# Kernel tuning notes

Hardware: AMD Instinct MI355X
Metric: run time of the kernel (lower is better)

The kernel has to match this reference:

```python
import math
import jax, jax.numpy as jnp
import numpy as np

B, T, D = 8, 2048, 512
EPS = 1e-5


def _gate(x, W, b, a, g, beta):
    # Linear -> PReLU (single shared slope a) -> LayerNorm -> sigmoid
    h = x @ W.T + b
    h = jnp.where(h >= 0, h, a * h)
    mu = jnp.mean(h, axis=-1, keepdims=True)
    var = jnp.var(h, axis=-1, keepdims=True)
    h = (h - mu) / jnp.sqrt(var + EPS) * g + beta
    return jax.nn.sigmoid(h)


def setup_inputs() -> dict:
    key = jax.random.key(0)
    ks = jax.random.split(key, 12)
    lin = lambda k: jax.random.normal(k, (D, D), jnp.float32) * 0.02
    z = jnp.zeros((D,), jnp.float32)
    o = jnp.ones((D,), jnp.float32)
    a0 = jnp.float32(0.25)  # PReLU default init
    inp = {
        "query": jax.random.normal(ks[0], (B, T, D), jnp.float32),
        "value": jax.random.normal(ks[1], (B, T, D), jnp.float32),
        "aux_emb": jax.random.normal(ks[2], (B, 1, D), jnp.float32),
        # ragged valid lengths in [T//2, T] to keep every sample realistic
        "input_len": jax.random.randint(ks[3], (B,), T // 2, T + 1),
        "Wq": lin(ks[4]), "bq": z,
        "Wqg": lin(ks[5]), "bqg": z, "aq": a0, "gq": o, "betaq": z,
        "Wkg": lin(ks[6]), "bkg": z, "ak": a0, "gk": o, "betak": z,
        "Wvg": lin(ks[7]), "bvg": z, "av": a0, "gv": o, "betav": z,
        "Wsig": lin(ks[8]), "bsig": z,
        "Wtan": lin(ks[9]), "btan": z,
    }
    return inp


def reference(query, value, aux_emb, input_len,
              Wq, bq,
              Wqg, bqg, aq, gq, betaq,
              Wkg, bkg, ak, gk, betak,
              Wvg, bvg, av, gv, betav,
              Wsig, bsig, Wtan, btan):
    q = query @ Wq.T + bq
    q = q * _gate(aux_emb, Wqg, bqg, aq, gq, betaq)          # [B,T,D]
    k = value * _gate(aux_emb, Wkg, bkg, ak, gk, betak)      # [B,T,D]
    vg = _gate(aux_emb, Wvg, bvg, av, gv, betav)             # [B,1,D]
    vg = jax.nn.sigmoid(vg @ Wsig.T + bsig) * jnp.tanh(vg @ Wtan.T + btan)
    v = value * vg                                           # [B,T,D]

    w = jnp.einsum('btd,bsd->bts', q, k) / math.sqrt(D)      # [B,T,T]
    r = jnp.arange(T)
    causal = (r[:, None] >= r[None, :]).astype(w.dtype)      # tril ones
    w = w * causal
    w = jnp.where(w == 0.0, -jnp.inf, w)  # torch quirk: exact zeros -> -inf
    L = input_len[:, None, None]                              # [B,1,1]
    invalid = (r[None, :, None] < L) & (r[None, None, :] >= L)
    w = jnp.where(invalid, -jnp.inf, w)
    p = jax.nn.softmax(w, axis=-1)
    # rows beyond input_len are padding: zero them (torch code produced NaN
    # there via -inf*0; intended semantics is zeroed padding rows)
    row_valid = (r[None, :, None] < L).astype(p.dtype)        # [B,T,1]
    p = p * row_valid
    return p @ v                                              # [B,T,D]
```

## Files before the change

### kernel.cpp

```cpp
#include <hip/hip_runtime.h>
#include <hip/hip_bf16.h>
#include <stdint.h>

#define BB 8
#define TT 2048
#define DD 512

typedef __attribute__((ext_vector_type(8))) __bf16 bf16x8;
typedef __attribute__((ext_vector_type(4))) float f32x4;

__device__ __forceinline__ unsigned short f2bf(float f) {
    unsigned u = __builtin_bit_cast(unsigned, f);
    unsigned r = u + 0x7fffu + ((u >> 16) & 1u);
    return (unsigned short)(r >> 16);
}

__device__ __forceinline__ void gload_lds16(const unsigned short* g, unsigned short* l) {
    __builtin_amdgcn_global_load_lds(
        (const __attribute__((address_space(1))) void*)g,
        (__attribute__((address_space(3))) void*)l, 16, 0, 0);
}

__global__ __launch_bounds__(256) void gates_mv1(
    const float* __restrict__ aux,
    const float* __restrict__ Wqg, const float* __restrict__ bqg, const float* __restrict__ aq,
    const float* __restrict__ Wkg, const float* __restrict__ bkg, const float* __restrict__ ak,
    const float* __restrict__ Wvg, const float* __restrict__ bvg, const float* __restrict__ av,
    float* __restrict__ h) {
    __shared__ float saux[BB * DD];
    int tid = threadIdx.x;
#pragma unroll
    for (int i = 0; i < 4; i++) {
        int idx = tid + i * 256;
        ((float4*)saux)[idx] = ((const float4*)aux)[idx];
    }
    __syncthreads();
    int wave = (blockIdx.x * 256 + tid) >> 6;
    int lane = tid & 63;
    int g = wave >> 9, r = wave & 511;
    const float* W    = (g == 0) ? Wqg : (g == 1) ? Wkg : Wvg;
    const float* bias = (g == 0) ? bqg : (g == 1) ? bkg : bvg;
    const float* alpha = (g == 0) ? aq : (g == 1) ? ak : av;
    const float4* Wrow = (const float4*)(W + (size_t)r * DD);
    float acc[BB];
#pragma unroll
    for (int b = 0; b < BB; b++) acc[b] = 0.f;
#pragma unroll
    for (int c = 0; c < 2; c++) {
        float4 w4 = Wrow[lane + c * 64];
#pragma unroll
        for (int b = 0; b < BB; b++) {
            float4 a4 = ((const float4*)(saux + b * DD))[lane + c * 64];
            acc[b] += w4.x * a4.x + w4.y * a4.y + w4.z * a4.z + w4.w * a4.w;
        }
    }
#pragma unroll
    for (int b = 0; b < BB; b++) {
#pragma unroll
        for (int s = 1; s < 64; s <<= 1) acc[b] += __shfl_xor(acc[b], s, 64);
    }
    if (lane == 0) {
        float bi = bias[r], a = alpha[0];
#pragma unroll
        for (int b = 0; b < BB; b++) {
            float v = acc[b] + bi;
            v = (v >= 0.f) ? v : a * v;
            h[(g * BB + b) * DD + r] = v;
        }
    }
}

__global__ __launch_bounds__(512) void gates_norm(
    const float* __restrict__ h,
    const float* __restrict__ gq, const float* __restrict__ betaq,
    const float* __restrict__ gk, const float* __restrict__ betak,
    const float* __restrict__ gv, const float* __restrict__ betav,
    float* __restrict__ qgate, float* __restrict__ kgate, float* __restrict__ vg) {
    int g = blockIdx.x >> 3, b = blockIdx.x & 7, tid = threadIdx.x;
    __shared__ float red[DD], red2[DD];
    float hv = h[(g * BB + b) * DD + tid];
    red[tid] = hv; red2[tid] = hv * hv;
    __syncthreads();
    for (int s = 256; s > 0; s >>= 1) {
        if (tid < s) { red[tid] += red[tid + s]; red2[tid] += red2[tid + s]; }
        __syncthreads();
    }
    float mu = red[0] * (1.f / DD);
    float var = red2[0] * (1.f / DD) - mu * mu;
    const float* gg = (g == 0) ? gq : (g == 1) ? gk : gv;
    const float* be = (g == 0) ? betaq : (g == 1) ? betak : betav;
    float val = (hv - mu) * rsqrtf(var + 1e-5f) * gg[tid] + be[tid];
    float sg = 1.f / (1.f + expf(-val));
    float* outp = (g == 0) ? qgate : (g == 1) ? kgate : vg;
    outp[b * DD + tid] = sg;
}

__global__ __launch_bounds__(256) void gates_mv2(
    const float* __restrict__ vg,
    const float* __restrict__ Wsig, const float* __restrict__ bsig,
    const float* __restrict__ Wtan, const float* __restrict__ btan,
    float* __restrict__ vgate) {
    __shared__ float svg[BB * DD];
    int tid = threadIdx.x;
#pragma unroll
    for (int i = 0; i < 4; i++) {
        int idx = tid + i * 256;
        ((float4*)svg)[idx] = ((const float4*)vg)[idx];
    }
    __syncthreads();
    int r = (blockIdx.x * 256 + tid) >> 6;
    int lane = tid & 63;
    const float4* Ws = (const float4*)(Wsig + (size_t)r * DD);
    const float4* Wt = (const float4*)(Wtan + (size_t)r * DD);
    float as_[BB], at_[BB];
#pragma unroll
    for (int b = 0; b < BB; b++) { as_[b] = 0.f; at_[b] = 0.f; }
#pragma unroll
    for (int c = 0; c < 2; c++) {
        float4 w1 = Ws[lane + c * 64];
        float4 w2 = Wt[lane + c * 64];
#pragma unroll
        for (int b = 0; b < BB; b++) {
            float4 a4 = ((const float4*)(svg + b * DD))[lane + c * 64];
            as_[b] += w1.x * a4.x + w1.y * a4.y + w1.z * a4.z + w1.w * a4.w;
            at_[b] += w2.x * a4.x + w2.y * a4.y + w2.z * a4.z + w2.w * a4.w;
        }
    }
#pragma unroll
    for (int b = 0; b < BB; b++) {
#pragma unroll
        for (int s = 1; s < 64; s <<= 1) {
            as_[b] += __shfl_xor(as_[b], s, 64);
            at_[b] += __shfl_xor(at_[b], s, 64);
        }
    }
    if (lane == 0) {
        float b1 = bsig[r], b2 = btan[r];
#pragma unroll
        for (int b = 0; b < BB; b++) {
            float s1 = 1.f / (1.f + expf(-(as_[b] + b1)));
            float s2 = tanhf(at_[b] + b2);
            vgate[b * DD + r] = s1 * s2;
        }
    }
}

__global__ __launch_bounds__(256) void convert_kernel(
    const float* __restrict__ query, const float* __restrict__ Wq,
    const float* __restrict__ value,
    const float* __restrict__ kgate, const float* __restrict__ vgate,
    unsigned short* __restrict__ queryb, unsigned short* __restrict__ Wqb,
    unsigned short* __restrict__ kb, unsigned short* __restrict__ vbT) {
    __shared__ float tile[32][33];
    int bi = blockIdx.x, tid = threadIdx.x;
    if (bi < 8192) {
        int idx = bi * 256 + tid;
        float4 q4 = ((const float4*)query)[idx];
        ushort4 oq;
        oq.x = f2bf(q4.x); oq.y = f2bf(q4.y); oq.z = f2bf(q4.z); oq.w = f2bf(q4.w);
        ((ushort4*)queryb)[idx] = oq;
    } else if (bi < 8448) {
        int idx = (bi - 8192) * 256 + tid;
        float4 w4 = ((const float4*)Wq)[idx];
        ushort4 o;
        o.x = f2bf(w4.x); o.y = f2bf(w4.y); o.z = f2bf(w4.z); o.w = f2bf(w4.w);
        ((ushort4*)Wqb)[idx] = o;
    } else {
        int vb = bi - 8448;
        int tIdx = vb & 63, dIdx = (vb >> 6) & 15, b = vb >> 10;
        int t0 = tIdx * 32, d0 = dIdx * 32;
        int tx = tid & 31, ty = tid >> 5;
        float kg = kgate[b * DD + d0 + tx];
#pragma unroll
        for (int i = 0; i < 4; i++) {
            int t = t0 + ty + i * 8;
            float v = value[((size_t)b * TT + t) * DD + d0 + tx];
            tile[ty + i * 8][tx] = v;
            kb[((size_t)b * TT + t) * DD + d0 + tx] = f2bf(v * kg);
        }
        __syncthreads();
#pragma unroll
        for (int i = 0; i < 4; i++) {
            int d = d0 + ty + i * 8;
            float g = vgate[b * DD + d];
            vbT[((size_t)b * DD + d) * TT + t0 + tx] = f2bf(tile[tx][ty + i * 8] * g);
        }
    }
}

#define GEMM_CORE(APTR, ALDA, BPTR, BLDA, KSTART, KEND)                                   \
    __shared__ __align__(16) unsigned short As[128 * 32];                                 \
    __shared__ __align__(16) unsigned short Bs[128 * 32];                                 \
    int tid = threadIdx.x;                                                                \
    int lane = tid & 63, wid = tid >> 6;                                                  \
    int wm = (wid >> 1) * 64, wn = (wid & 1) * 64;                                        \
    int lm = lane & 15, quad = lane >> 4;                                                 \
    f32x4 acc[4][4];                                                                      \
    _Pragma("unroll") for (int im = 0; im < 4; im++)                                      \
        _Pragma("unroll") for (int in = 0; in < 4; in++)                                  \
            acc[im][in] = (f32x4){0.f, 0.f, 0.f, 0.f};                                    \
    for (int k0 = (KSTART); k0 < (KEND); k0 += 32) {                                      \
        _Pragma("unroll") for (int i = 0; i < 2; i++) {                                   \
            int idx = tid * 8 + i * 2048;                                                 \
            int r = idx >> 5;                                                             \
            int cg = ((idx >> 3) & 3) ^ ((r >> 1) & 3);                                   \
            gload_lds16(&(APTR)[(size_t)r * (ALDA) + k0 + cg * 8], &As[idx]);             \
            gload_lds16(&(BPTR)[(size_t)r * (BLDA) + k0 + cg * 8], &Bs[idx]);             \
        }                                                                                 \
        __syncthreads();                                                                  \
        bf16x8 af[4], bf_[4];                                                             \
        _Pragma("unroll") for (int i = 0; i < 4; i++) {                                   \
            int row = wm + i * 16 + lm;                                                   \
            af[i] = *(const bf16x8*)&As[row * 32 + (quad ^ ((row >> 1) & 3)) * 8];        \
        }                                                                                 \
        _Pragma("unroll") for (int i = 0; i < 4; i++) {                                   \
            int row = wn + i * 16 + lm;                                                   \
            bf_[i] = *(const bf16x8*)&Bs[row * 32 + (quad ^ ((row >> 1) & 3)) * 8];       \
        }                                                                                 \
        _Pragma("unroll") for (int im = 0; im < 4; im++)                                  \
            _Pragma("unroll") for (int in = 0; in < 4; in++)                              \
                acc[im][in] = __builtin_amdgcn_mfma_f32_16x16x32_bf16(af[im], bf_[in],    \
                                                                     acc[im][in], 0, 0, 0);\
        __syncthreads();                                                                  \
    }

__global__ __launch_bounds__(256) void qgemm_kernel(
    const unsigned short* __restrict__ Amat, const unsigned short* __restrict__ Bmat,
    const float* __restrict__ bq, const float* __restrict__ qgate,
    unsigned short* __restrict__ qb) {
    int m0 = blockIdx.x * 128, n0 = blockIdx.y * 128;
    const unsigned short* Ap = Amat + (size_t)m0 * DD;
    const unsigned short* Bp = Bmat + (size_t)n0 * DD;
    GEMM_CORE(Ap, DD, Bp, DD, 0, DD)
    int b = m0 >> 11;
#pragma unroll
    for (int im = 0; im < 4; im++) {
        int row = m0 + wm + im * 16 + quad * 4;
#pragma unroll
        for (int in = 0; in < 4; in++) {
            int col = n0 + wn + in * 16 + lm;
            float bias = bq[col];
            float g = qgate[b * DD + col];
#pragma unroll
            for (int r = 0; r < 4; r++) {
                float v = (acc[im][in][r] + bias) * g;
                qb[(size_t)(row + r) * DD + col] = f2bf(v);
            }
        }
    }
}

__global__ __launch_bounds__(256) void scores_kernel(
    const unsigned short* __restrict__ qb, const unsigned short* __restrict__ kb,
    unsigned short* __restrict__ P, float* __restrict__ rowsum) {
    int b = blockIdx.z;
    int idx = blockIdx.x;
    int mt = (int)((sqrtf(8.f * idx + 1.f) - 1.f) * 0.5f);
    while ((mt + 1) * (mt + 2) / 2 <= idx) mt++;
    while (mt * (mt + 1) / 2 > idx) mt--;
    int nt = idx - mt * (mt + 1) / 2;
    int t0 = mt * 128, s0 = nt * 128;
    const unsigned short* Ap = qb + ((size_t)b * TT + t0) * DD;
    const unsigned short* Bp = kb + ((size_t)b * TT + s0) * DD;
    GEMM_CORE(Ap, DD, Bp, DD, 0, DD)
    const float scale = 0.044194173824159216f;
    unsigned short* Ptile = P + ((size_t)b * 136 + (size_t)mt * (mt + 1) / 2 + nt) * 16384;
#pragma unroll
    for (int im = 0; im < 4; im++) {
        int ltb = wm + im * 16 + quad * 4;
        float rs[4] = {0.f, 0.f, 0.f, 0.f};
#pragma unroll
        for (int in = 0; in < 4; in++) {
            int ls = wn + in * 16 + lm;
            int s = s0 + ls;
#pragma unroll
            for (int r = 0; r < 4; r++) {
                float p = (s <= t0 + ltb + r) ? expf(acc[im][in][r] * scale) : 0.f;
                Ptile[(size_t)(ltb + r) * 128 + ls] = f2bf(p);
                rs[r] += p;
            }
        }
#pragma unroll
        for (int r = 0; r < 4; r++) {
            float v = rs[r];
            v += __shfl_xor(v, 1, 64);
            v += __shfl_xor(v, 2, 64);
            v += __shfl_xor(v, 4, 64);
            v += __shfl_xor(v, 8, 64);
            if (lm == 0) atomicAdd(&rowsum[b * TT + t0 + ltb + r], v);
        }
    }
}

__global__ __launch_bounds__(256) void out_kernel(
    const unsigned short* __restrict__ P, const unsigned short* __restrict__ vbT,
    const float* __restrict__ rowsum, const int* __restrict__ input_len,
    float* __restrict__ out) {
    int nt = blockIdx.x;
    int pr = blockIdx.y;
    int b = blockIdx.z;
    int n0 = nt * 128;
    int L = input_len[b];

    __shared__ __align__(16) unsigned short As[64 * 64];
    __shared__ __align__(16) unsigned short Bs[128 * 64];
    int tid = threadIdx.x;
    int lane = tid & 63, wid = tid >> 6;
    int wm = (wid >> 1) * 32, wn = (wid & 1) * 64;
    int lm = lane & 15, quad = lane >> 4;

#pragma unroll
    for (int half = 0; half < 2; half++) {
        int mt = half ? (31 - pr) : pr;
        int t0 = mt * 64;
        int mt128 = mt >> 1;
        int rowoff = (mt & 1) * 64;
        size_t triBase = ((size_t)b * 136 + (size_t)mt128 * (mt128 + 1) / 2) * 16384;
        int ksteps = mt + 1;

        f32x4 acc[2][4];
#pragma unroll
        for (int im = 0; im < 2; im++)
#pragma unroll
            for (int in = 0; in < 4; in++) acc[im][in] = (f32x4){0.f, 0.f, 0.f, 0.f};

        for (int ks = 0; ks < ksteps; ks++) {
            int k0 = ks * 64;
            int stile = k0 >> 7;
            int coloff = k0 & 64;
#pragma unroll
            for (int i = 0; i < 2; i++) {
                int idx = tid * 8 + i * 2048;
                int r = idx >> 6;
                int c = (idx >> 3) & 7;
                int cs = c ^ (r & 7);
                const unsigned short* ag = P + triBase + (size_t)stile * 16384 +
                                           (size_t)(rowoff + r) * 128 + coloff + cs * 8;
                gload_lds16(ag, &As[idx]);
            }
#pragma unroll
            for (int i = 0; i < 4; i++) {
                int idx = tid * 8 + i * 2048;
                int r = idx >> 6;
                int c = (idx >> 3) & 7;
                int cs = c ^ (r & 7);
                gload_lds16(&vbT[(size_t)(b * DD + n0 + r) * TT + k0 + cs * 8], &Bs[idx]);
            }
            __syncthreads();
            bf16x8 af[2][2], bf_[4][2];
#pragma unroll
            for (int kk = 0; kk < 2; kk++) {
#pragma unroll
                for (int i = 0; i < 2; i++) {
                    int row = wm + i * 16 + lm;
                    af[i][kk] = *(const bf16x8*)&As[row * 64 + ((kk * 4 + quad) ^ (row & 7)) * 8];
                }
#pragma unroll
                for (int i = 0; i < 4; i++) {
                    int row = wn + i * 16 + lm;
                    bf_[i][kk] = *(const bf16x8*)&Bs[row * 64 + ((kk * 4 + quad) ^ (row & 7)) * 8];
                }
            }
#pragma unroll
            for (int kk = 0; kk < 2; kk++)
#pragma unroll
                for (int im = 0; im < 2; im++)
#pragma unroll
                    for (int in = 0; in < 4; in++)
                        acc[im][in] = __builtin_amdgcn_mfma_f32_16x16x32_bf16(
                            af[im][kk], bf_[in][kk], acc[im][in], 0, 0, 0);
            __syncthreads();
        }

#pragma unroll
        for (int im = 0; im < 2; im++) {
            int tbase = t0 + wm + im * 16 + quad * 4;
#pragma unroll
            for (int r = 0; r < 4; r++) {
                int t = tbase + r;
                float inv = 1.f / rowsum[b * TT + t];
                bool valid = (t < L);
#pragma unroll
                for (int in = 0; in < 4; in++) {
                    int n = n0 + wn + in * 16 + lm;
                    float o = valid ? acc[im][in][r] * inv : 0.f;
                    out[((size_t)b * TT + t) * DD + n] = o;
                }
            }
        }
    }
}

extern "C" void kernel_launch(void* const* d_in, const int* in_sizes, int n_in,
                              void* d_out, int out_size, void* d_ws, size_t ws_size,
                              hipStream_t stream) {
    const float* query = (const float*)d_in[0];
    const float* value = (const float*)d_in[1];
    const float* aux   = (const float*)d_in[2];
    const int*   ilen  = (const int*)d_in[3];
    const float* Wq    = (const float*)d_in[4];
    const float* bq    = (const float*)d_in[5];
    const float* Wqg   = (const float*)d_in[6];
    const float* bqg   = (const float*)d_in[7];
    const float* aq    = (const float*)d_in[8];
    const float* gq    = (const float*)d_in[9];
    const float* betaq = (const float*)d_in[10];
    const float* Wkg   = (const float*)d_in[11];
    const float* bkg   = (const float*)d_in[12];
    const float* ak    = (const float*)d_in[13];
    const float* gk    = (const float*)d_in[14];
    const float* betak = (const float*)d_in[15];
    const float* Wvg   = (const float*)d_in[16];
    const float* bvg   = (const float*)d_in[17];
    const float* av    = (const float*)d_in[18];
    const float* gv    = (const float*)d_in[19];
    const float* betav = (const float*)d_in[20];
    const float* Wsig  = (const float*)d_in[21];
    const float* bsig  = (const float*)d_in[22];
    const float* Wtan  = (const float*)d_in[23];
    const float* btan  = (const float*)d_in[24];

    char* ws = (char*)d_ws;
    float* qgate          = (float*)(ws + 0);
    float* kgate          = (float*)(ws + 16384);
    float* vgate          = (float*)(ws + 32768);
    float* rowsum         = (float*)(ws + 49152);
    unsigned short* Wqb   = (unsigned short*)(ws + 114688);
    unsigned short* queryb= (unsigned short*)(ws + 638976);
    unsigned short* qb    = (unsigned short*)(ws + 17416192);
    unsigned short* kb    = (unsigned short*)(ws + 34193408);
    unsigned short* vbT   = (unsigned short*)(ws + 50970624);
    unsigned short* P     = (unsigned short*)(ws + 67747840);
    float* hbuf           = (float*)(ws + 67747840);
    float* vg             = (float*)(ws + 67747840 + 49152);

    hipMemsetAsync(rowsum, 0, BB * TT * sizeof(float), stream);

    gates_mv1<<<384, 256, 0, stream>>>(aux, Wqg, bqg, aq, Wkg, bkg, ak, Wvg, bvg, av, hbuf);
    gates_norm<<<24, 512, 0, stream>>>(hbuf, gq, betaq, gk, betak, gv, betav,
                                       qgate, kgate, vg);
    gates_mv2<<<128, 256, 0, stream>>>(vg, Wsig, bsig, Wtan, btan, vgate);

    convert_kernel<<<16640, 256, 0, stream>>>(query, Wq, value, kgate, vgate,
                                              queryb, Wqb, kb, vbT);
    qgemm_kernel<<<dim3((BB * TT) / 128, DD / 128), 256, 0, stream>>>(queryb, Wqb, bq, qgate, qb);
    scores_kernel<<<dim3(136, 1, BB), 256, 0, stream>>>(qb, kb, P, rowsum);
    out_kernel<<<dim3(4, 16, BB), 256, 0, stream>>>(P, vbT, rowsum, ilen, (float*)d_out);
}
```

Before: 275.1 us.

## Double-buffer LDS tiles in GEMM core and output kernel to overlap loads

Both the shared GEMM macro and the P@V output kernel now use two LDS buffers. The next k-tile is prefetched with global_load_lds right after the barrier, while MFMAs run on the current tile, and the trailing barrier per iteration is removed. The goal is to hide global-memory latency behind compute. In exchange, LDS use doubles, which can lower occupancy. Dropping the end-of-iteration barrier also relies on the single top barrier to prevent a write-after-read race on the buffer being refilled, and that ordering looks fragile.

```diff
diff --git a/kernel.cpp b/kernel.cpp
--- a/kernel.cpp
+++ b/kernel.cpp
@@ -188,9 +188,21 @@
     }
 }
 
+#define STAGE_AB(BUF, K0)                                                                 \
+    _Pragma("unroll") for (int i = 0; i < 2; i++) {                                       \
+        int idx = tid * 8 + i * 2048;                                                     \
+        int r = idx >> 5;                                                                 \
+        int cg = ((idx >> 3) & 3) ^ ((r >> 1) & 3);                                       \
+        gload_lds16(&Ap_[(size_t)r * lda_ + (K0) + cg * 8], &As[BUF][idx]);               \
+        gload_lds16(&Bp_[(size_t)r * ldb_ + (K0) + cg * 8], &Bs[BUF][idx]);               \
+    }
+
 #define GEMM_CORE(APTR, ALDA, BPTR, BLDA, KSTART, KEND)                                   \
-    __shared__ __align__(16) unsigned short As[128 * 32];                                 \
-    __shared__ __align__(16) unsigned short Bs[128 * 32];                                 \
+    __shared__ __align__(16) unsigned short As[2][128 * 32];                              \
+    __shared__ __align__(16) unsigned short Bs[2][128 * 32];                              \
+    const unsigned short* Ap_ = (APTR);                                                   \
+    const unsigned short* Bp_ = (BPTR);                                                   \
+    const int lda_ = (ALDA), ldb_ = (BLDA);                                               \
     int tid = threadIdx.x;                                                                \
     int lane = tid & 63, wid = tid >> 6;                                                  \
     int wm = (wid >> 1) * 64, wn = (wid & 1) * 64;                                        \
@@ -199,29 +211,25 @@
     _Pragma("unroll") for (int im = 0; im < 4; im++)                                      \
         _Pragma("unroll") for (int in = 0; in < 4; in++)                                  \
             acc[im][in] = (f32x4){0.f, 0.f, 0.f, 0.f};                                    \
+    STAGE_AB(0, (KSTART))                                                                 \
+    int cur_ = 0;                                                                         \
     for (int k0 = (KSTART); k0 < (KEND); k0 += 32) {                                      \
-        _Pragma("unroll") for (int i = 0; i < 2; i++) {                                   \
-            int idx = tid * 8 + i * 2048;                                                 \
-            int r = idx >> 5;                                                             \
-            int cg = ((idx >> 3) & 3) ^ ((r >> 1) & 3);                                   \
-            gload_lds16(&(APTR)[(size_t)r * (ALDA) + k0 + cg * 8], &As[idx]);             \
-            gload_lds16(&(BPTR)[(size_t)r * (BLDA) + k0 + cg * 8], &Bs[idx]);             \
-        }                                                                                 \
         __syncthreads();                                                                  \
+        if (k0 + 32 < (KEND)) { STAGE_AB(cur_ ^ 1, k0 + 32) }                             \
         bf16x8 af[4], bf_[4];                                                             \
         _Pragma("unroll") for (int i = 0; i < 4; i++) {                                   \
             int row = wm + i * 16 + lm;                                                   \
-            af[i] = *(const bf16x8*)&As[row * 32 + (quad ^ ((row >> 1) & 3)) * 8];        \
+            af[i] = *(const bf16x8*)&As[cur_][row * 32 + (quad ^ ((row >> 1) & 3)) * 8];  \
         }                                                                                 \
         _Pragma("unroll") for (int i = 0; i < 4; i++) {                                   \
             int row = wn + i * 16 + lm;                                                   \
-            bf_[i] = *(const bf16x8*)&Bs[row * 32 + (quad ^ ((row >> 1) & 3)) * 8];       \
+            bf_[i] = *(const bf16x8*)&Bs[cur_][row * 32 + (quad ^ ((row >> 1) & 3)) * 8]; \
         }                                                                                 \
         _Pragma("unroll") for (int im = 0; im < 4; im++)                                  \
             _Pragma("unroll") for (int in = 0; in < 4; in++)                              \
                 acc[im][in] = __builtin_amdgcn_mfma_f32_16x16x32_bf16(af[im], bf_[in],    \
                                                                      acc[im][in], 0, 0, 0);\
-        __syncthreads();                                                                  \
+        cur_ ^= 1;                                                                        \
     }
 
 __global__ __launch_bounds__(256) void qgemm_kernel(
@@ -302,8 +310,8 @@
     int n0 = nt * 128;
     int L = input_len[b];
 
-    __shared__ __align__(16) unsigned short As[64 * 64];
-    __shared__ __align__(16) unsigned short Bs[128 * 64];
+    __shared__ __align__(16) unsigned short As[2][64 * 64];
+    __shared__ __align__(16) unsigned short Bs[2][128 * 64];
     int tid = threadIdx.x;
     int lane = tid & 63, wid = tid >> 6;
     int wm = (wid >> 1) * 32, wn = (wid & 1) * 64;
@@ -324,41 +332,47 @@
 #pragma unroll
             for (int in = 0; in < 4; in++) acc[im][in] = (f32x4){0.f, 0.f, 0.f, 0.f};
 
+#define OUT_STAGE(BUF, KS)                                                              \
+        {                                                                               \
+            int k0s = (KS) * 64;                                                        \
+            int stile = k0s >> 7;                                                       \
+            int coloff = k0s & 64;                                                      \
+            _Pragma("unroll") for (int i = 0; i < 2; i++) {                             \
+                int idx = tid * 8 + i * 2048;                                           \
+                int r = idx >> 6;                                                       \
+                int c = (idx >> 3) & 7;                                                 \
+                int cs = c ^ (r & 7);                                                   \
+                const unsigned short* ag = P + triBase + (size_t)stile * 16384 +        \
+                                           (size_t)(rowoff + r) * 128 + coloff + cs * 8;\
+                gload_lds16(ag, &As[BUF][idx]);                                         \
+            }                                                                           \
+            _Pragma("unroll") for (int i = 0; i < 4; i++) {                             \
+                int idx = tid * 8 + i * 2048;                                           \
+                int r = idx >> 6;                                                       \
+                int c = (idx >> 3) & 7;                                                 \
+                int cs = c ^ (r & 7);                                                   \
+                gload_lds16(&vbT[(size_t)(b * DD + n0 + r) * TT + k0s + cs * 8],        \
+                            &Bs[BUF][idx]);                                             \
+            }                                                                           \
+        }
+
+        OUT_STAGE(0, 0)
+        int cur = 0;
         for (int ks = 0; ks < ksteps; ks++) {
-            int k0 = ks * 64;
-            int stile = k0 >> 7;
-            int coloff = k0 & 64;
-#pragma unroll
-            for (int i = 0; i < 2; i++) {
-                int idx = tid * 8 + i * 2048;
-                int r = idx >> 6;
-                int c = (idx >> 3) & 7;
-                int cs = c ^ (r & 7);
-                const unsigned short* ag = P + triBase + (size_t)stile * 16384 +
-                                           (size_t)(rowoff + r) * 128 + coloff + cs * 8;
-                gload_lds16(ag, &As[idx]);
-            }
-#pragma unroll
-            for (int i = 0; i < 4; i++) {
-                int idx = tid * 8 + i * 2048;
-                int r = idx >> 6;
-                int c = (idx >> 3) & 7;
-                int cs = c ^ (r & 7);
-                gload_lds16(&vbT[(size_t)(b * DD + n0 + r) * TT + k0 + cs * 8], &Bs[idx]);
-            }
             __syncthreads();
+            if (ks + 1 < ksteps) { OUT_STAGE(cur ^ 1, ks + 1) }
             bf16x8 af[2][2], bf_[4][2];
 #pragma unroll
             for (int kk = 0; kk < 2; kk++) {
 #pragma unroll
                 for (int i = 0; i < 2; i++) {
                     int row = wm + i * 16 + lm;
-                    af[i][kk] = *(const bf16x8*)&As[row * 64 + ((kk * 4 + quad) ^ (row & 7)) * 8];
+                    af[i][kk] = *(const bf16x8*)&As[cur][row * 64 + ((kk * 4 + quad) ^ (row & 7)) * 8];
                 }
 #pragma unroll
                 for (int i = 0; i < 4; i++) {
                     int row = wn + i * 16 + lm;
-                    bf_[i][kk] = *(const bf16x8*)&Bs[row * 64 + ((kk * 4 + quad) ^ (row & 7)) * 8];
+                    bf_[i][kk] = *(const bf16x8*)&Bs[cur][row * 64 + ((kk * 4 + quad) ^ (row & 7)) * 8];
                 }
             }
 #pragma unroll
@@ -369,8 +383,10 @@
                     for (int in = 0; in < 4; in++)
                         acc[im][in] = __builtin_amdgcn_mfma_f32_16x16x32_bf16(
                             af[im][kk], bf_[in][kk], acc[im][in], 0, 0, 0);
-            __syncthreads();
-        }
+            cur ^= 1;
+        }
+        __syncthreads();
+#undef OUT_STAGE
 
 #pragma unroll
         for (int im = 0; im < 2; im++) {
```

Measured after the change: 273.2 us. Within noise of the previous version (-0.7%).
